# Optimization experiments

Measured on AMD Instinct MI355X. Metric: run time of the kernel, lower is better.

Reference implementation:

```python
import jax, jax.numpy as jnp
import numpy as np

B, S, D, H = 2, 2048, 1024, 16
HD = D // H  # head_dim = 64


def setup_inputs() -> dict:
    key = jax.random.key(0)
    k1, k2, k3 = jax.random.split(key, 3)
    inputs = jax.random.normal(k1, (B, S, D), dtype=jnp.float32)
    segment_positions = jnp.broadcast_to(jnp.arange(S, dtype=jnp.int32), (B, S))
    # causal boolean mask, broadcast over batch and heads: [1,1,S,S]
    mask = jnp.tril(jnp.ones((S, S), dtype=bool))[None, None]
    W_in = jax.random.normal(k2, (D, 3 * D), dtype=jnp.float32) * (D ** -0.5)
    W_out = jax.random.normal(k3, (D, D), dtype=jnp.float32) * (D ** -0.5)
    return {"inputs": inputs, "segment_positions": segment_positions,
            "mask": mask, "W_in": W_in, "W_out": W_out}


def _rope(x, pos):
    # x: [B,S,H,HD], pos: [B,S] int. Rotate-half RoPE with base 10000.
    half = HD // 2
    inv_freq = 1.0 / (10000.0 ** (jnp.arange(half, dtype=jnp.float32) / half))
    ang = pos[..., None].astype(jnp.float32) * inv_freq          # [B,S,half]
    cos = jnp.cos(ang)[:, :, None, :]                             # [B,S,1,half]
    sin = jnp.sin(ang)[:, :, None, :]
    x1, x2 = jnp.split(x, 2, axis=-1)
    return jnp.concatenate([x1 * cos - x2 * sin, x1 * sin + x2 * cos], axis=-1)


def reference(inputs, segment_positions, mask, W_in, W_out):
    # fused QKV projection: [B,S,3D] -> [B,S,H,3*HD] -> chunk into q,k,v
    qkv = (inputs @ W_in).reshape(B, S, H, 3 * HD)
    q, k, v = jnp.split(qkv, 3, axis=-1)                          # each [B,S,H,HD]
    q = _rope(q, segment_positions)
    k = _rope(k, segment_positions)
    q = q / jnp.sqrt(jnp.asarray(HD, q.dtype))
    scores = jnp.einsum('bqhd,bkhd->bhqk', q, k)                  # [B,H,S,S]
    big_neg = jnp.finfo(scores.dtype).min
    scores = jnp.where(mask, scores, big_neg)
    attn = jax.nn.softmax(scores, axis=-1)
    x = jnp.einsum('bhqk,bkhd->bqhd', attn, v).reshape(B, S, D)
    return x @ W_out
```

## Files before the change

kernel.cpp:

```cpp
#include <hip/hip_runtime.h>

typedef unsigned short u16;
typedef __bf16 bf16x8 __attribute__((ext_vector_type(8)));
typedef float f32x4 __attribute__((ext_vector_type(4)));

__device__ __forceinline__ float b2f(u16 x) {
    union { float f; unsigned u; } v; v.u = ((unsigned)x) << 16; return v.f;
}
__device__ __forceinline__ u16 f2b(float f) {
    union { float f; unsigned u; } v; v.f = f;
    unsigned u = v.u;
    return (u16)((u + 0x7FFFu + ((u >> 16) & 1u)) >> 16);
}
__device__ __forceinline__ unsigned pk2(float a, float b) {
    unsigned ua = __float_as_uint(a), ub = __float_as_uint(b);
    return (ub & 0xFFFF0000u) | (ua >> 16);
}
__device__ __forceinline__ f32x4 mfma_16x16x32(bf16x8 a, bf16x8 b, f32x4 c) {
    return __builtin_amdgcn_mfma_f32_16x16x32_bf16(a, b, c, 0, 0, 0);
}
__device__ __forceinline__ void gld_lds16(const u16* g, u16* l) {
    __builtin_amdgcn_global_load_lds(
        (const __attribute__((address_space(1))) unsigned int*)g,
        (__attribute__((address_space(3))) unsigned int*)l,
        16, 0, 0);
}

#define VSTRIDE 2080
#define LOG2E 1.44269504f

__global__ __launch_bounds__(256) void prep(const float* __restrict__ inputs,
                                            u16* __restrict__ inB,
                                            const float* __restrict__ W_in,
                                            u16* __restrict__ WtB,
                                            const float* __restrict__ W_out,
                                            u16* __restrict__ WotB) {
    __shared__ float T[32][33];
    const int bx = blockIdx.x;
    if (bx < 4096) {
        int i = (bx * 256 + threadIdx.x) * 4;
        float4 v = *(const float4*)(inputs + i);
        ushort4 o;
        o.x = f2b(v.x); o.y = f2b(v.y); o.z = f2b(v.z); o.w = f2b(v.w);
        *(ushort4*)(inB + i) = o;
        return;
    }
    const float* src; u16* dst; int R, C, c0, r0;
    if (bx < 7168) {
        int t = bx - 4096; src = W_in; dst = WtB; R = 1024; C = 3072;
        c0 = (t % 96) * 32; r0 = (t / 96) * 32;
    } else {
        int t = bx - 7168; src = W_out; dst = WotB; R = 1024; C = 1024;
        c0 = (t % 32) * 32; r0 = (t / 32) * 32;
    }
    int tr = threadIdx.x >> 5, tc = threadIdx.x & 31;
#pragma unroll
    for (int p = 0; p < 4; ++p)
        T[tr + p * 8][tc] = src[(size_t)(r0 + tr + p * 8) * C + c0 + tc];
    __syncthreads();
#pragma unroll
    for (int p = 0; p < 4; ++p)
        dst[(size_t)(c0 + tr + p * 8) * R + r0 + tc] = f2b(T[tc][tr + p * 8]);
}

template <bool F32OUT>
__global__ __launch_bounds__(256) void gemm_tn(const u16* __restrict__ A,
                                               const u16* __restrict__ Bt,
                                               void* __restrict__ Cv,
                                               int M, int N, int K) {
    __shared__ u16 As[128 * 32];
    __shared__ u16 Bs[128 * 32];
    const int tid = threadIdx.x;
    const int m0 = blockIdx.y * 128;
    const int n0 = blockIdx.x * 128;
    const int w = tid >> 6, lane = tid & 63;
    const int col16 = lane & 15, quad = lane >> 4;
    const int wm = (w >> 1) * 64, wn = (w & 1) * 64;
    const int srow = (lane >> 2), sseg = (lane & 3) * 8;

    f32x4 acc[4][4];
#pragma unroll
    for (int i = 0; i < 4; ++i)
#pragma unroll
        for (int j = 0; j < 4; ++j) acc[i][j] = (f32x4){0.f, 0.f, 0.f, 0.f};

    for (int kt = 0; kt < K; kt += 32) {
#pragma unroll
        for (int cc = 0; cc < 2; ++cc) {
            int c = w * 2 + cc;
            int row = c * 16 + srow;
            gld_lds16(A + (size_t)(m0 + row) * K + kt + sseg, &As[c * 512 + lane * 8]);
            gld_lds16(Bt + (size_t)(n0 + row) * K + kt + sseg, &Bs[c * 512 + lane * 8]);
        }
        __syncthreads();

        bf16x8 af[4], bfr[4];
#pragma unroll
        for (int i = 0; i < 4; ++i)
            af[i] = *(const bf16x8*)&As[(wm + i * 16 + col16) * 32 + quad * 8];
#pragma unroll
        for (int j = 0; j < 4; ++j)
            bfr[j] = *(const bf16x8*)&Bs[(wn + j * 16 + col16) * 32 + quad * 8];
#pragma unroll
        for (int i = 0; i < 4; ++i)
#pragma unroll
            for (int j = 0; j < 4; ++j)
                acc[i][j] = mfma_16x16x32(af[i], bfr[j], acc[i][j]);
        __syncthreads();
    }

#pragma unroll
    for (int i = 0; i < 4; ++i) {
#pragma unroll
        for (int r = 0; r < 4; ++r) {
            int m = m0 + wm + i * 16 + quad * 4 + r;
            if (F32OUT) {
                float* Crow = (float*)Cv + (size_t)m * N + n0 + wn;
#pragma unroll
                for (int j = 0; j < 4; ++j)
                    Crow[j * 16 + col16] = acc[i][j][r];
            } else {
                u16* Crow = (u16*)Cv + (size_t)m * N + n0 + wn;
#pragma unroll
                for (int j = 0; j < 4; ++j)
                    Crow[j * 16 + col16] = f2b(acc[i][j][r]);
            }
        }
    }
}

__global__ __launch_bounds__(256) void rope_vt(const u16* __restrict__ qkv,
                                               const int* __restrict__ segpos,
                                               u16* __restrict__ Qh,
                                               u16* __restrict__ Kh,
                                               u16* __restrict__ Vt) {
    __shared__ u16 T[32][72];
    const int bx = blockIdx.x;
    if (bx < 1024) {
        int t = bx * 256 + threadIdx.x;
        int seg = t & 3;
        int h = (t >> 2) & 15;
        int row = t >> 6;
        float pos = (float)segpos[row];
        const u16* base = qkv + (size_t)row * 3072 + h * 192 + seg * 8;
        union { uint4 u; u16 s[8]; } q1, q2, k1, k2, oq1, oq2, ok1, ok2;
        q1.u = *(const uint4*)(base);
        q2.u = *(const uint4*)(base + 32);
        k1.u = *(const uint4*)(base + 64);
        k2.u = *(const uint4*)(base + 96);
        const float qs = 0.125f * LOG2E;
#pragma unroll
        for (int j = 0; j < 8; ++j) {
            int d = seg * 8 + j;
            float inv_freq = __expf(-(float)d * (9.210340371976184f / 32.0f));
            float ang = pos * inv_freq;
            float c = __cosf(ang), s = __sinf(ang);
            float a1 = b2f(q1.s[j]), a2 = b2f(q2.s[j]);
            float b1 = b2f(k1.s[j]), b2v = b2f(k2.s[j]);
            oq1.s[j] = f2b((a1 * c - a2 * s) * qs);
            oq2.s[j] = f2b((a1 * s + a2 * c) * qs);
            ok1.s[j] = f2b(b1 * c - b2v * s);
            ok2.s[j] = f2b(b1 * s + b2v * c);
        }
        int b = row >> 11, srow = row & 2047;
        size_t idx = ((size_t)(b * 16 + h) * 2048 + srow) * 64 + seg * 8;
        *(uint4*)&Qh[idx]      = oq1.u;
        *(uint4*)&Qh[idx + 32] = oq2.u;
        *(uint4*)&Kh[idx]      = ok1.u;
        *(uint4*)&Kh[idx + 32] = ok2.u;
        return;
    }
    int bxx = bx - 1024;
    int s0 = (bxx & 63) * 32;
    int bh = bxx >> 6;
    int b = bh >> 4, h = bh & 15;
    int t = threadIdx.x;
    {
        int r = t >> 3, seg = t & 7;
        const u16* src = qkv + (size_t)(b * 2048 + s0 + r) * 3072 + h * 192 + 128 + seg * 8;
        *(uint4*)&T[r][seg * 8] = *(const uint4*)src;
    }
    __syncthreads();
    {
        int d = t >> 2, ss = (t & 3) * 8;
        union { uint4 u; u16 s[8]; } w;
#pragma unroll
        for (int j = 0; j < 8; ++j) w.s[j] = T[ss + j][d];
        *(uint4*)(Vt + (size_t)bh * 64 * VSTRIDE + (size_t)d * VSTRIDE + s0 + ss) = w.u;
    }
}

#define FIXED_M2 34.6246561f

__global__ __launch_bounds__(256) void attn_v8(const u16* __restrict__ Qh,
                                               const u16* __restrict__ Kh,
                                               const u16* __restrict__ Vt,
                                               u16* __restrict__ X) {
    __shared__ u16 Ks[2][64 * 64];
    __shared__ u16 Vs[2][64 * 64];
    __shared__ u16 Ps[4][32 * 64];
    __shared__ float lred[4][32];
    const int tid = threadIdx.x;
    const int w = tid >> 6, lane = tid & 63;
    const int col16 = lane & 15, quad = lane >> 4;
    const int raw = blockIdx.x;
    const int tileq = 15 - (raw >> 5);
    const int bh = raw & 31;
    const int q0 = tileq * 128 + w * 32;
    const u16* Qp = Qh + (size_t)bh * 2048 * 64;
    const u16* Kp = Kh + (size_t)bh * 2048 * 64;
    const u16* Vp = Vt + (size_t)bh * 64 * VSTRIDE;
    u16* Pw = Ps[w];
    const int swz = (col16 & 7) << 3;

    bf16x8 qa[2][2];
#pragma unroll
    for (int t = 0; t < 2; ++t)
#pragma unroll
        for (int hf = 0; hf < 2; ++hf)
            qa[t][hf] = *(const bf16x8*)&Qp[(size_t)(q0 + t * 16 + col16) * 64 + hf * 32 + quad * 8];

    float l_acc[2] = {0.f, 0.f};
    f32x4 o[2][4];
#pragma unroll
    for (int t = 0; t < 2; ++t)
#pragma unroll
        for (int f = 0; f < 4; ++f) o[t][f] = (f32x4){0.f, 0.f, 0.f, 0.f};

    const int sr = lane >> 3;
    const int sg = ((lane & 7) ^ sr) * 8;
    const int nchunk = 2 * (tileq + 1);

#pragma unroll
    for (int i = 0; i < 2; ++i) {
        int c = w * 2 + i;
        gld_lds16(Kp + (size_t)(c * 8 + sr) * 64 + sg, &Ks[0][c * 512 + lane * 8]);
    }
#pragma unroll
    for (int i = 0; i < 2; ++i) {
        int c = w * 2 + i;
        gld_lds16(Vp + (size_t)(c * 8 + sr) * VSTRIDE + sg, &Vs[0][c * 512 + lane * 8]);
    }

    for (int ci = 0; ci < nchunk; ++ci) {
        const int cur = ci & 1;
        const u16* KsC = Ks[cur];
        const u16* VsC = Vs[cur];

        if (ci + 1 < nchunk) {
            const int k0n = (ci + 1) * 64;
            u16* Kd = Ks[cur ^ 1];
            u16* Vd = Vs[cur ^ 1];
#pragma unroll
            for (int i = 0; i < 2; ++i) {
                int c = w * 2 + i;
                gld_lds16(Kp + (size_t)(k0n + c * 8 + sr) * 64 + sg, Kd + c * 512 + lane * 8);
            }
#pragma unroll
            for (int i = 0; i < 2; ++i) {
                int c = w * 2 + i;
                gld_lds16(Vp + (size_t)(c * 8 + sr) * VSTRIDE + k0n + sg, Vd + c * 512 + lane * 8);
            }
            asm volatile("s_waitcnt vmcnt(4)" ::: "memory");
        } else {
            asm volatile("s_waitcnt vmcnt(0)" ::: "memory");
        }
        asm volatile("s_barrier" ::: "memory");

        const int k0 = ci * 64;

        f32x4 s[2][4];
#pragma unroll
        for (int t = 0; t < 2; ++t)
#pragma unroll
            for (int kt = 0; kt < 4; ++kt) s[t][kt] = (f32x4){0.f, 0.f, 0.f, 0.f};
#pragma unroll
        for (int kt = 0; kt < 4; ++kt) {
            const u16* kb = &KsC[(kt * 16 + col16) * 64];
            bf16x8 kf0 = *(const bf16x8*)&kb[(quad * 8) ^ swz];
            bf16x8 kf1 = *(const bf16x8*)&kb[(32 + quad * 8) ^ swz];
            s[0][kt] = mfma_16x16x32(kf0, qa[0][0], s[0][kt]);
            s[0][kt] = mfma_16x16x32(kf1, qa[0][1], s[0][kt]);
            s[1][kt] = mfma_16x16x32(kf0, qa[1][0], s[1][kt]);
            s[1][kt] = mfma_16x16x32(kf1, qa[1][1], s[1][kt]);
        }

        const bool domask = (k0 + 63 > q0);
#pragma unroll
        for (int t = 0; t < 2; ++t) {
            const int qg = q0 + t * 16 + col16;
            float rs = 0.f;
#pragma unroll
            for (int kt = 0; kt < 4; ++kt) {
                float p[4];
#pragma unroll
                for (int r = 0; r < 4; ++r) {
                    float sv = s[t][kt][r];
                    if (domask && (k0 + kt * 16 + quad * 4 + r > qg)) sv = -1e30f;
                    p[r] = __builtin_amdgcn_exp2f(sv - FIXED_M2);
                    rs += p[r];
                }
                unsigned* prow = (unsigned*)&Pw[(t * 16 + col16) * 64 + ((kt * 16 + quad * 4) ^ swz)];
                prow[0] = pk2(p[0], p[1]);
                prow[1] = pk2(p[2], p[3]);
            }
            l_acc[t] += rs;
        }
        asm volatile("s_waitcnt lgkmcnt(0)" ::: "memory");

#pragma unroll
        for (int ss = 0; ss < 2; ++ss) {
            const int ko = (ss * 32 + quad * 8) ^ swz;
            bf16x8 pf0 = *(const bf16x8*)&Pw[(col16) * 64 + ko];
            bf16x8 pf1 = *(const bf16x8*)&Pw[(16 + col16) * 64 + ko];
#pragma unroll
            for (int f = 0; f < 4; ++f) {
                bf16x8 vf = *(const bf16x8*)&VsC[(f * 16 + col16) * 64 + ko];
                o[0][f] = mfma_16x16x32(pf0, vf, o[0][f]);
                o[1][f] = mfma_16x16x32(pf1, vf, o[1][f]);
            }
        }
        asm volatile("s_waitcnt lgkmcnt(0)" ::: "memory");
        asm volatile("s_barrier" ::: "memory");
    }

#pragma unroll
    for (int t = 0; t < 2; ++t) {
        float l = l_acc[t];
        l += __shfl_xor(l, 16);
        l += __shfl_xor(l, 32);
        if (quad == 0) lred[w][t * 16 + col16] = l;
    }
    asm volatile("s_waitcnt lgkmcnt(0)" ::: "memory");

    const int b = bh >> 4, h = bh & 15;
#pragma unroll
    for (int t = 0; t < 2; ++t) {
#pragma unroll
        for (int r = 0; r < 4; ++r) {
            float inv = 1.0f / lred[w][t * 16 + quad * 4 + r];
            int srow = q0 + t * 16 + quad * 4 + r;
            u16* Xp = X + ((size_t)(b * 2048 + srow)) * 1024 + h * 64;
#pragma unroll
            for (int f = 0; f < 4; ++f)
                Xp[f * 16 + col16] = f2b(o[t][f][r] * inv);
        }
    }
}

extern "C" void kernel_launch(void* const* d_in, const int* in_sizes, int n_in,
                              void* d_out, int out_size, void* d_ws, size_t ws_size,
                              hipStream_t stream) {
    const float* inputs = (const float*)d_in[0];
    const int* segpos   = (const int*)d_in[1];
    const float* W_in   = (const float*)d_in[3];
    const float* W_out  = (const float*)d_in[4];
    float* out = (float*)d_out;

    u16* ws = (u16*)d_ws;
    u16* qkv   = ws;
    u16* x     = qkv;
    u16* inB   = qkv + 12582912 + 512;
    u16* WtB   = inB + 4194304 + 512;
    u16* WotB  = WtB + 3145728 + 512;
    u16* Qh    = WotB + 1048576 + 512;
    u16* Kh    = Qh + 4194304 + 512;
    u16* Vt    = Kh + 4194304 + 512;

    prep<<<dim3(8192), 256, 0, stream>>>(inputs, inB, W_in, WtB, W_out, WotB);
    gemm_tn<false><<<dim3(24, 32), 256, 0, stream>>>(inB, WtB, qkv, 4096, 3072, 1024);
    rope_vt<<<dim3(3072), 256, 0, stream>>>(qkv, segpos, Qh, Kh, Vt);
    attn_v8<<<dim3(512), 256, 0, stream>>>(Qh, Kh, Vt, x);
    gemm_tn<true><<<dim3(8, 32), 256, 0, stream>>>(x, WotB, out, 4096, 1024, 1024);
}
```

Measured before the change: 229.0 us.

## Split long causal attention tiles across KV ranges and reduce partials separately

Causal attention work is redistributed from 512 query-tile blocks of very uneven length into 864 blocks, each capped at 14 KV chunks. Lookup tables map every block to a query tile, a starting KV chunk and a chunk count. Blocks that cover only part of a long tile write unnormalised fp32 partial outputs and row sums to workspace. A new reduce kernel sums these partials and normalises them. This relies on the fixed softmax max, so partials can be added without rescaling. It aims to remove tail imbalance across CUs, at the cost of an extra launch and extra fp32 partial traffic.

```diff
diff --git a/kernel.cpp b/kernel.cpp
--- a/kernel.cpp
+++ b/kernel.cpp
@@ -192,10 +192,20 @@
 
 #define FIXED_M2 34.6246561f
 
-__global__ __launch_bounds__(256) void attn_v8(const u16* __restrict__ Qh,
+__device__ const int UTQ[27] = {6,7,8,9,10,11,12,13,13,14,14,15,15, 5,12, 4,11, 3,10, 2,9, 1,8,15, 0,7,14};
+__device__ const int UK0[27] = {0,0,0,0,0,0,0,0,14,0,14,0,14, 0,14, 0,14, 0,14, 0,14, 0,14,28, 0,14,28};
+__device__ const int UNC[27] = {14,14,14,14,14,14,14,14,14,14,14,14,14, 12,12, 10,10, 8,8, 6,6, 4,4,4, 2,2,2};
+__device__ const int UPS[27] = {-1,0,1,2,3,4,5,6,7,8,9,10,11, -1,12, -1,13, -1,14, -1,15, -1,16,17, -1,18,19};
+__device__ const int RUN[9]    = {2,2,2,2,2,2,2,3,3};
+__device__ const int RUS[9][3] = {{0,18,-1},{1,16,-1},{2,15,-1},{3,14,-1},{4,13,-1},
+                                  {5,12,-1},{6,7,-1},{8,9,19},{10,11,17}};
+
+__global__ __launch_bounds__(256) void attn_v9(const u16* __restrict__ Qh,
                                                const u16* __restrict__ Kh,
                                                const u16* __restrict__ Vt,
-                                               u16* __restrict__ X) {
+                                               u16* __restrict__ X,
+                                               float* __restrict__ Opart,
+                                               float* __restrict__ Lpart) {
     __shared__ u16 Ks[2][64 * 64];
     __shared__ u16 Vs[2][64 * 64];
     __shared__ u16 Ps[4][32 * 64];
@@ -204,9 +214,14 @@
     const int w = tid >> 6, lane = tid & 63;
     const int col16 = lane & 15, quad = lane >> 4;
     const int raw = blockIdx.x;
-    const int tileq = 15 - (raw >> 5);
-    const int bh = raw & 31;
-    const int q0 = tileq * 128 + w * 32;
+    const int bsw = (raw & 7) * 108 + (raw >> 3);
+    const int bh = bsw / 27;
+    const int slot = bsw - bh * 27;
+    const int tq = UTQ[slot];
+    const int c0 = UK0[slot];
+    const int nc = UNC[slot];
+    const int ps = UPS[slot];
+    const int q0 = tq * 128 + w * 32;
     const u16* Qp = Qh + (size_t)bh * 2048 * 64;
     const u16* Kp = Kh + (size_t)bh * 2048 * 64;
     const u16* Vp = Vt + (size_t)bh * 64 * VSTRIDE;
@@ -229,26 +244,28 @@
 
     const int sr = lane >> 3;
     const int sg = ((lane & 7) ^ sr) * 8;
-    const int nchunk = 2 * (tileq + 1);
-
-#pragma unroll
-    for (int i = 0; i < 2; ++i) {
-        int c = w * 2 + i;
-        gld_lds16(Kp + (size_t)(c * 8 + sr) * 64 + sg, &Ks[0][c * 512 + lane * 8]);
-    }
-#pragma unroll
-    for (int i = 0; i < 2; ++i) {
-        int c = w * 2 + i;
-        gld_lds16(Vp + (size_t)(c * 8 + sr) * VSTRIDE + sg, &Vs[0][c * 512 + lane * 8]);
-    }
-
-    for (int ci = 0; ci < nchunk; ++ci) {
+
+    {
+        const int k0 = c0 * 64;
+#pragma unroll
+        for (int i = 0; i < 2; ++i) {
+            int c = w * 2 + i;
+            gld_lds16(Kp + (size_t)(k0 + c * 8 + sr) * 64 + sg, &Ks[0][c * 512 + lane * 8]);
+        }
+#pragma unroll
+        for (int i = 0; i < 2; ++i) {
+            int c = w * 2 + i;
+            gld_lds16(Vp + (size_t)(c * 8 + sr) * VSTRIDE + k0 + sg, &Vs[0][c * 512 + lane * 8]);
+        }
+    }
+
+    for (int ci = 0; ci < nc; ++ci) {
         const int cur = ci & 1;
         const u16* KsC = Ks[cur];
         const u16* VsC = Vs[cur];
 
-        if (ci + 1 < nchunk) {
-            const int k0n = (ci + 1) * 64;
+        if (ci + 1 < nc) {
+            const int k0n = (c0 + ci + 1) * 64;
             u16* Kd = Ks[cur ^ 1];
             u16* Vd = Vs[cur ^ 1];
 #pragma unroll
@@ -267,7 +284,7 @@
         }
         asm volatile("s_barrier" ::: "memory");
 
-        const int k0 = ci * 64;
+        const int k0 = (c0 + ci) * 64;
 
         f32x4 s[2][4];
 #pragma unroll
@@ -324,14 +341,37 @@
         asm volatile("s_barrier" ::: "memory");
     }
 
+    float lt[2];
 #pragma unroll
     for (int t = 0; t < 2; ++t) {
         float l = l_acc[t];
         l += __shfl_xor(l, 16);
         l += __shfl_xor(l, 32);
+        lt[t] = l;
         if (quad == 0) lred[w][t * 16 + col16] = l;
     }
     asm volatile("s_waitcnt lgkmcnt(0)" ::: "memory");
+
+    if (ps >= 0) {
+        const int pg = bh * 20 + ps;
+        float* Op = Opart + ((size_t)pg * 128 + w * 32) * 64;
+#pragma unroll
+        for (int t = 0; t < 2; ++t) {
+#pragma unroll
+            for (int r = 0; r < 4; ++r) {
+                float* Crow = Op + (t * 16 + quad * 4 + r) * 64;
+#pragma unroll
+                for (int f = 0; f < 4; ++f)
+                    Crow[f * 16 + col16] = o[t][f][r];
+            }
+        }
+        if (quad == 0) {
+            float* Lp = Lpart + (size_t)pg * 128 + w * 32;
+#pragma unroll
+            for (int t = 0; t < 2; ++t) Lp[t * 16 + col16] = lt[t];
+        }
+        return;
+    }
 
     const int b = bh >> 4, h = bh & 15;
 #pragma unroll
@@ -345,6 +385,42 @@
             for (int f = 0; f < 4; ++f)
                 Xp[f * 16 + col16] = f2b(o[t][f][r] * inv);
         }
+    }
+}
+
+__global__ __launch_bounds__(256) void attn_reduce(const float* __restrict__ Opart,
+                                                   const float* __restrict__ Lpart,
+                                                   u16* __restrict__ X) {
+    const int bh = blockIdx.x;
+    const int ti = blockIdx.y;
+    const int tq = 7 + ti;
+    const int tid = threadIdx.x;
+    const int b = bh >> 4, h = bh & 15;
+    const int np = RUN[ti];
+    const size_t g0 = (size_t)(bh * 20 + RUS[ti][0]);
+    const size_t g1 = (size_t)(bh * 20 + RUS[ti][1]);
+    const size_t g2 = (np > 2) ? (size_t)(bh * 20 + RUS[ti][2]) : 0;
+    const float4* O0 = (const float4*)Opart + g0 * 2048;
+    const float4* O1 = (const float4*)Opart + g1 * 2048;
+    const float4* O2 = (const float4*)Opart + g2 * 2048;
+#pragma unroll
+    for (int i = 0; i < 8; ++i) {
+        int e4 = i * 256 + tid;
+        int q = e4 >> 4, d0 = (e4 & 15) * 4;
+        float4 a = O0[e4];
+        float4 c = O1[e4];
+        a.x += c.x; a.y += c.y; a.z += c.z; a.w += c.w;
+        float l = Lpart[g0 * 128 + q] + Lpart[g1 * 128 + q];
+        if (np > 2) {
+            float4 d = O2[e4];
+            a.x += d.x; a.y += d.y; a.z += d.z; a.w += d.w;
+            l += Lpart[g2 * 128 + q];
+        }
+        float inv = 1.0f / l;
+        ushort4 ov;
+        ov.x = f2b(a.x * inv); ov.y = f2b(a.y * inv);
+        ov.z = f2b(a.z * inv); ov.w = f2b(a.w * inv);
+        *(ushort4*)&X[((size_t)(b * 2048 + tq * 128 + q)) * 1024 + h * 64 + d0] = ov;
     }
 }
 
@@ -366,10 +442,13 @@
     u16* Qh    = WotB + 1048576 + 512;
     u16* Kh    = Qh + 4194304 + 512;
     u16* Vt    = Kh + 4194304 + 512;
+    float* Opart = (float*)(ws + 8388608);
+    float* Lpart = (float*)(ws + 8388608 + 10485760);
 
     prep<<<dim3(8192), 256, 0, stream>>>(inputs, inB, W_in, WtB, W_out, WotB);
     gemm_tn<false><<<dim3(24, 32), 256, 0, stream>>>(inB, WtB, qkv, 4096, 3072, 1024);
     rope_vt<<<dim3(3072), 256, 0, stream>>>(qkv, segpos, Qh, Kh, Vt);
-    attn_v8<<<dim3(512), 256, 0, stream>>>(Qh, Kh, Vt, x);
+    attn_v9<<<dim3(864), 256, 0, stream>>>(Qh, Kh, Vt, x, Opart, Lpart);
+    attn_reduce<<<dim3(32, 9), 256, 0, stream>>>(Opart, Lpart, x);
     gemm_tn<true><<<dim3(8, 32), 256, 0, stream>>>(x, WotB, out, 4096, 1024, 1024);
 }
```

Result: faster. 213.4 us (-6.8%).
